# Kernel tuning notes

Hardware: AMD Instinct MI355X
Metric: run time of the kernel (lower is better)

## Reference

```python
import jax, jax.numpy as jnp
import numpy as np

N_NODES = 100000
N_EDGES = 1600000
IN_CH = 128
OUT_CH = 64

def setup_inputs() -> dict:
    key = jax.random.key(0)
    k = jax.random.split(key, 7)
    x = jax.random.normal(k[0], (N_NODES, IN_CH), dtype=jnp.float32)
    edge_index = jax.random.randint(k[1], (2, N_EDGES), 0, N_NODES, dtype=jnp.int64)
    neg_edge_index = jax.random.randint(k[2], (2, N_EDGES), 0, N_NODES, dtype=jnp.int64)
    # GCNConv weight [in, out] + bias, Linear classifier [2*out, 2] + bias
    W = jax.random.normal(k[3], (IN_CH, OUT_CH), dtype=jnp.float32) / np.sqrt(IN_CH)
    b = jnp.zeros((OUT_CH,), dtype=jnp.float32)
    Wc = jax.random.normal(k[4], (2 * OUT_CH, 2), dtype=jnp.float32) / np.sqrt(2 * OUT_CH)
    bc = jnp.zeros((2,), dtype=jnp.float32)
    return {"x": x, "edge_index": edge_index, "neg_edge_index": neg_edge_index,
            "W": W, "b": b, "Wc": Wc, "bc": bc}

def reference(x, edge_index, neg_edge_index, W, b, Wc, bc):
    N = x.shape[0]
    # --- GCNConv: linear transform, add self-loops, symmetric deg normalization ---
    h = x @ W                                   # [N, out]
    loops = jnp.arange(N, dtype=edge_index.dtype)
    row = jnp.concatenate([edge_index[0], loops])   # source
    col = jnp.concatenate([edge_index[1], loops])   # target
    deg = jax.ops.segment_sum(jnp.ones(col.shape, h.dtype), col, num_segments=N)
    dinv = jnp.where(deg > 0, jax.lax.rsqrt(deg), 0.0)
    norm = dinv[row] * dinv[col]                # [E+N]
    agg = jax.ops.segment_sum(h[row] * norm[:, None], col, num_segments=N)
    z = jax.nn.relu(agg + b)                    # [N, out]
    # --- edge feature gather (pos + neg edges) + linear classifier ---
    total = jnp.concatenate([edge_index, neg_edge_index], axis=1)  # [2, 2E]
    feats = jnp.concatenate([z[total[0]], z[total[1]]], axis=1)    # [2E, 2*out]
    return feats @ Wc + bc                      # [2E, 2]
```

## Files before the change

kernel.cpp:

```cpp
#include <hip/hip_runtime.h>

#define IN_CH 128
#define OUT_CH 64
#define MAXBKT 256
#define CAPB   9216
#define CAPB_PAD 16896
#define CHUNK  3328

typedef __attribute__((ext_vector_type(8))) short short8v;
typedef __attribute__((ext_vector_type(4))) float float4v;

union Pack { short8v s8; unsigned u[4]; };

__device__ __forceinline__ unsigned short f2bf(float f) {
    unsigned u = __float_as_uint(f);
    return (unsigned short)((u + 0x7fffu + ((u >> 16) & 1u)) >> 16);
}
__device__ __forceinline__ unsigned pk2(float a, float b) {
    return ((unsigned)f2bf(b) << 16) | (unsigned)f2bf(a);
}
__device__ __forceinline__ float bflo(unsigned d) { return __uint_as_float(d << 16); }
__device__ __forceinline__ float bfhi(unsigned d) { return __uint_as_float(d & 0xffff0000u); }

__global__ void k_zero_cnt(unsigned* __restrict__ cnt, int n) {
    int i = blockIdx.x * blockDim.x + threadIdx.x;
    if (i < n) cnt[i] = 0u;
}

__global__ __launch_bounds__(256) void k_binA(const int* __restrict__ ei,
                                              unsigned* __restrict__ bucketCount,
                                              unsigned* __restrict__ binned,
                                              int E, int nbkt) {
    __shared__ unsigned hist[MAXBKT];
    __shared__ unsigned resv[MAXBKT];
    __shared__ int colS[CHUNK];
    int tid = threadIdx.x;
    int start = blockIdx.x * CHUNK;
    int end = start + CHUNK; if (end > E) end = E;
    int cnt = end - start;

    for (int i = tid; i < MAXBKT; i += 256) hist[i] = 0u;
    __syncthreads();

    for (int i = tid; i < cnt; i += 256) {
        int c = ei[E + start + i];
        colS[i] = c;
        atomicAdd(&hist[c >> 9], 1u);
    }
    __syncthreads();

    if (tid < nbkt) {
        resv[tid] = atomicAdd(&bucketCount[tid], hist[tid]);
        hist[tid] = 0u;
    }
    __syncthreads();

    for (int i = tid; i < cnt; i += 256) {
        int c = colS[i];
        int r = ei[start + i];
        int bkt = c >> 9;
        unsigned rank = atomicAdd(&hist[bkt], 1u);
        unsigned idx = resv[bkt] + rank;
        if (idx < CAPB)
            binned[(size_t)bkt * CAPB + idx] = ((unsigned)r << 9) | (unsigned)(c & 511);
    }
}

__global__ __launch_bounds__(1024) void k_csrB(const unsigned* __restrict__ binned,
                                               const unsigned* __restrict__ bucketCount,
                                               int* __restrict__ rows,
                                               unsigned* __restrict__ offs,
                                               unsigned* __restrict__ degPad,
                                               float* __restrict__ dinv, int N, int nbkt) {
    __shared__ unsigned hist[512];
    __shared__ unsigned excl[512];
    __shared__ unsigned wsum[8];
    __shared__ unsigned wexc[8];
    __shared__ unsigned stage[CAPB];
    int tid = threadIdx.x;
    int b = blockIdx.x;
    unsigned cnt = bucketCount[b];
    if (cnt > (unsigned)CAPB) cnt = (unsigned)CAPB;
    size_t gbase = (size_t)b * CAPB_PAD;
    int nodeBase = b << 9;
    int nn = N - nodeBase; if (nn > 512) nn = 512;

    for (int i = tid; i < 512; i += 1024) hist[i] = 0u;
    __syncthreads();

    const unsigned* src = binned + (size_t)b * CAPB;
    for (unsigned i = tid; i < cnt; i += 1024) {
        unsigned p = src[i];
        stage[i] = p;
        atomicAdd(&hist[p & 511u], 1u);
    }
    __syncthreads();

    unsigned d = 0, dp = 0, winc = 0;
    if (tid < 512) {
        d = hist[tid];
        dp = (d + 15u) & ~15u;
        winc = dp;
#pragma unroll
        for (int o = 1; o < 64; o <<= 1) {
            unsigned t = __shfl_up(winc, o);
            if ((tid & 63) >= o) winc += t;
        }
        if ((tid & 63) == 63) wsum[tid >> 6] = winc;
    }
    __syncthreads();
    if (tid < 8) {
        unsigned s = wsum[tid];
        unsigned inc = s;
#pragma unroll
        for (int o = 1; o < 8; o <<= 1) {
            unsigned t = __shfl_up(inc, o);
            if (tid >= o) inc += t;
        }
        wexc[tid] = inc - s;
    }
    __syncthreads();
    if (tid < 512) excl[tid] = wexc[tid >> 6] + winc - dp;
    __syncthreads();

    if (tid < nn) {
        offs[nodeBase + tid]   = (unsigned)gbase + excl[tid];
        degPad[nodeBase + tid] = dp;
        dinv[nodeBase + tid]   = rsqrtf((float)d + 1.0f);
    }

    for (unsigned i = tid; i < cnt; i += 1024) {
        unsigned p = stage[i];
        unsigned c = p & 511u;
        unsigned r = atomicAdd(&hist[c], 0xFFFFFFFFu);
        rows[gbase + excl[c] + r - 1u] = (int)(p >> 9);
    }
    if (tid < nn) {
        size_t base = gbase + excl[tid];
        for (unsigned p = d; p < dp; ++p) rows[base + p] = N;
    }
}

__global__ __launch_bounds__(256) void k_gemm_h(const float* __restrict__ x,
                                                const float* __restrict__ W,
                                                const float* __restrict__ dinv,
                                                unsigned short* __restrict__ hs,
                                                int N, int nChunks) {
    __shared__ float Wl[IN_CH * 66];
    int tid = threadIdx.x;
    int wid = tid >> 6;
    int l   = tid & 63;
    int g   = l >> 4;
    int m   = l & 15;

    if (blockIdx.x == 0 && tid < 32)
        ((unsigned*)hs)[((size_t)N << 5) + tid] = 0u;

    const float4* W4 = (const float4*)W;
#pragma unroll
    for (int j = 0; j < 8; ++j) {
        int i4 = tid + j * 256;
        float4 w = W4[i4];
        int i = i4 * 4;
        int k = i >> 6, c = i & 63;
        float* dst = Wl + k * 66 + c;
        dst[0] = w.x; dst[1] = w.y; dst[2] = w.z; dst[3] = w.w;
    }
    __syncthreads();

    short8v bf[4][4];
#pragma unroll
    for (int s = 0; s < 4; ++s)
#pragma unroll
        for (int t = 0; t < 4; ++t) {
            Pack p;
#pragma unroll
            for (int jj = 0; jj < 4; ++jj) {
                int k = s * 32 + g * 8 + 2 * jj;
                float f0 = Wl[(k + 0) * 66 + t * 16 + m];
                float f1 = Wl[(k + 1) * 66 + t * 16 + m];
                p.u[jj] = pk2(f0, f1);
            }
            bf[s][t] = p.s8;
        }

    const float4* x4 = (const float4*)x;
    for (int chunk = blockIdx.x; chunk < nChunks; chunk += gridDim.x) {
        int R0 = chunk * 64 + wid * 16;
        int rowA = R0 + m; if (rowA > N - 1) rowA = N - 1;
        float4v acc[4];
#pragma unroll
        for (int t = 0; t < 4; ++t) acc[t] = (float4v){0.f, 0.f, 0.f, 0.f};

#pragma unroll
        for (int s = 0; s < 4; ++s) {
            const float4* ap = x4 + (size_t)rowA * 32 + s * 8 + g * 2;
            float4 a0 = ap[0];
            float4 a1 = ap[1];
            Pack pa;
            pa.u[0] = pk2(a0.x, a0.y);
            pa.u[1] = pk2(a0.z, a0.w);
            pa.u[2] = pk2(a1.x, a1.y);
            pa.u[3] = pk2(a1.z, a1.w);
#pragma unroll
            for (int t = 0; t < 4; ++t)
                acc[t] = __builtin_amdgcn_mfma_f32_16x16x32_bf16(pa.s8, bf[s][t], acc[t], 0, 0, 0);
        }

        int rbase = R0 + g * 4;
        float4 dv = *(const float4*)(dinv + rbase);
#pragma unroll
        for (int r = 0; r < 4; ++r) {
            int row = rbase + r;
            if (row < N) {
                float dvr = (r == 0) ? dv.x : (r == 1) ? dv.y : (r == 2) ? dv.z : dv.w;
#pragma unroll
                for (int t = 0; t < 4; ++t)
                    hs[(size_t)row * OUT_CH + t * 16 + m] = f2bf(acc[t][r] * dvr);
            }
        }
    }
}

__global__ __launch_bounds__(256) void k_gather(const unsigned* __restrict__ offs,
                                                const unsigned* __restrict__ degPad,
                                                const int* __restrict__ rows,
                                                const unsigned* __restrict__ hsd,
                                                const float* __restrict__ dinv,
                                                const float* __restrict__ b,
                                                const float* __restrict__ Wc,
                                                float* __restrict__ u,
                                                float* __restrict__ v, int n) {
    int lane = threadIdx.x & 63;
    int half = lane >> 5;
    int l32  = lane & 31;
    int node = blockIdx.x * (blockDim.x >> 6) + (threadIdx.x >> 6);
    if (node >= n) return;
    unsigned start = offs[node];
    unsigned cntP = degPad[node];
    const int* rp = rows + start;

    unsigned ds = hsd[((size_t)node << 5) + l32];
    float acc0 = half ? 0.f : bflo(ds);
    float acc1 = half ? 0.f : bfhi(ds);

    for (unsigned j0 = 0; j0 < cntP; j0 += 64) {
        unsigned rem = cntP - j0;
        unsigned np = rem < 64u ? rem : 64u;
        int myidx = rp[j0 + (lane < (int)np ? lane : 0)];

        for (unsigned t0 = 0; t0 < np; t0 += 16) {
            int rr[8];
#pragma unroll
            for (int s = 0; s < 8; ++s)
                rr[s] = __shfl(myidx, (int)t0 + 2 * s + half);
            unsigned dd[8];
#pragma unroll
            for (int s = 0; s < 8; ++s)
                dd[s] = hsd[((size_t)rr[s] << 5) + l32];
#pragma unroll
            for (int s = 0; s < 8; ++s) {
                acc0 += bflo(dd[s]);
                acc1 += bfhi(dd[s]);
            }
        }
    }

    acc0 += __shfl_xor(acc0, 32);
    acc1 += __shfl_xor(acc1, 32);

    float di = dinv[node];
    float2 bv = ((const float2*)b)[l32];
    float z0 = fmaxf(fmaf(acc0, di, bv.x), 0.f);
    float z1 = fmaxf(fmaf(acc1, di, bv.y), 0.f);

    float4 w = ((const float4*)(Wc + (half ? 128 : 0)))[l32];
    float p0 = z0 * w.x + z1 * w.z;
    float p1 = z0 * w.y + z1 * w.w;
#pragma unroll
    for (int off = 16; off > 0; off >>= 1) {
        p0 += __shfl_xor(p0, off);
        p1 += __shfl_xor(p1, off);
    }
    float2 r; r.x = p0; r.y = p1;
    if (lane == 0)  ((float2*)u)[node] = r;
    if (lane == 32) ((float2*)v)[node] = r;
}

__global__ void k_edges(const int* __restrict__ ei, const int* __restrict__ nei,
                        const float* __restrict__ u, const float* __restrict__ v,
                        const float* __restrict__ bc, float* __restrict__ out, int E) {
    int i = blockIdx.x * blockDim.x + threadIdx.x;
    int quads = E >> 1;
    if (i >= quads) return;
    int halfQ = quads >> 1;
    const int* base = (i < halfQ) ? ei : nei;
    int pi = (i < halfQ) ? i : i - halfQ;
    int4 ss = ((const int4*)base)[pi];
    int4 dd = ((const int4*)(base + E))[pi];
    float2 u0 = ((const float2*)u)[ss.x];
    float2 u1 = ((const float2*)u)[ss.y];
    float2 u2 = ((const float2*)u)[ss.z];
    float2 u3 = ((const float2*)u)[ss.w];
    float2 v0 = ((const float2*)v)[dd.x];
    float2 v1 = ((const float2*)v)[dd.y];
    float2 v2 = ((const float2*)v)[dd.z];
    float2 v3 = ((const float2*)v)[dd.w];
    float b0 = bc[0], b1 = bc[1];
    float4 r0, r1;
    r0.x = u0.x + v0.x + b0;  r0.y = u0.y + v0.y + b1;
    r0.z = u1.x + v1.x + b0;  r0.w = u1.y + v1.y + b1;
    r1.x = u2.x + v2.x + b0;  r1.y = u2.y + v2.y + b1;
    r1.z = u3.x + v3.x + b0;  r1.w = u3.y + v3.y + b1;
    ((float4*)out)[2 * i + 0] = r0;
    ((float4*)out)[2 * i + 1] = r1;
}

extern "C" void kernel_launch(void* const* d_in, const int* in_sizes, int n_in,
                              void* d_out, int out_size, void* d_ws, size_t ws_size,
                              hipStream_t stream) {
    const float* x   = (const float*)d_in[0];
    const int*   ei  = (const int*)d_in[1];
    const int*   nei = (const int*)d_in[2];
    const float* W   = (const float*)d_in[3];
    const float* b   = (const float*)d_in[4];
    const float* Wc  = (const float*)d_in[5];
    const float* bc  = (const float*)d_in[6];
    float* out = (float*)d_out;

    const int N = in_sizes[0] / IN_CH;
    const int E = in_sizes[1] / 2;
    const int nbkt = (N + 511) >> 9;
    const int nChunks = (N + 63) / 64;

    char* ws = (char*)d_ws;
    size_t off = 0;
    unsigned short* hs = (unsigned short*)(ws + off); off += ((size_t)N + 1) * OUT_CH * 2;
    unsigned* binned = (unsigned*)(ws + off); off += (size_t)MAXBKT * CAPB * 4;
    int*      rows   = (int*)(ws + off);      off += (size_t)MAXBKT * CAPB_PAD * 4;
    unsigned* offs   = (unsigned*)(ws + off); off += (size_t)N * 4;
    unsigned* degP   = (unsigned*)(ws + off); off += (size_t)N * 4;
    float*    dinv   = (float*)(ws + off);    off += (size_t)N * 4;
    float*    u      = (float*)(ws + off);    off += (size_t)N * 2 * 4;
    float*    v      = (float*)(ws + off);    off += (size_t)N * 2 * 4;
    unsigned* bucketCount = (unsigned*)(ws + off); off += (size_t)MAXBKT * 4;

    k_zero_cnt<<<1, 256, 0, stream>>>(bucketCount, MAXBKT);
    k_binA<<<(E + CHUNK - 1) / CHUNK, 256, 0, stream>>>(ei, bucketCount, binned, E, nbkt);
    k_csrB<<<nbkt, 1024, 0, stream>>>(binned, bucketCount, rows, offs, degP, dinv, N, nbkt);
    k_gemm_h<<<512, 256, 0, stream>>>(x, W, dinv, hs, N, nChunks);
    k_gather<<<(N + 3) / 4, 256, 0, stream>>>(offs, degP, rows, (const unsigned*)hs, dinv, b, Wc, u, v, N);
    k_edges<<<(E / 2 + 255) / 256, 256, 0, stream>>>(ei, nei, u, v, bc, out, E);
}
```

Before: 137.7 us.

## Fuse edge binning with GEMM and defer dinv scaling into CSR kernel

Edge binning and the x@W GEMM now run in one launch, with blocks split by index, so the two independent stages overlap and one kernel launch goes away. Because the GEMM no longer waits for dinv, it writes unscaled bf16 h, and the CSR kernel rescales each node's row by dinv after computing degrees. The cost is an extra read-modify-write pass over hs in the CSR kernel and a second bf16 rounding. The GEMM also drops its grid-stride loop and launches one block per 64-row chunk, which repacks the W fragments in every block.

```diff
diff --git a/kernel.cpp b/kernel.cpp
--- a/kernel.cpp
+++ b/kernel.cpp
@@ -27,42 +27,120 @@
     if (i < n) cnt[i] = 0u;
 }
 
-__global__ __launch_bounds__(256) void k_binA(const int* __restrict__ ei,
-                                              unsigned* __restrict__ bucketCount,
-                                              unsigned* __restrict__ binned,
-                                              int E, int nbkt) {
-    __shared__ unsigned hist[MAXBKT];
-    __shared__ unsigned resv[MAXBKT];
-    __shared__ int colS[CHUNK];
+__global__ __launch_bounds__(256) void k_AG(const float* __restrict__ x,
+                                            const float* __restrict__ W,
+                                            const int* __restrict__ ei,
+                                            unsigned* __restrict__ bucketCount,
+                                            unsigned* __restrict__ binned,
+                                            unsigned short* __restrict__ hs,
+                                            int N, int E, int nbkt, int nBin) {
+    __shared__ float smem[IN_CH * 66];
     int tid = threadIdx.x;
-    int start = blockIdx.x * CHUNK;
-    int end = start + CHUNK; if (end > E) end = E;
-    int cnt = end - start;
-
-    for (int i = tid; i < MAXBKT; i += 256) hist[i] = 0u;
-    __syncthreads();
-
-    for (int i = tid; i < cnt; i += 256) {
-        int c = ei[E + start + i];
-        colS[i] = c;
-        atomicAdd(&hist[c >> 9], 1u);
-    }
-    __syncthreads();
-
-    if (tid < nbkt) {
-        resv[tid] = atomicAdd(&bucketCount[tid], hist[tid]);
-        hist[tid] = 0u;
-    }
-    __syncthreads();
-
-    for (int i = tid; i < cnt; i += 256) {
-        int c = colS[i];
-        int r = ei[start + i];
-        int bkt = c >> 9;
-        unsigned rank = atomicAdd(&hist[bkt], 1u);
-        unsigned idx = resv[bkt] + rank;
-        if (idx < CAPB)
-            binned[(size_t)bkt * CAPB + idx] = ((unsigned)r << 9) | (unsigned)(c & 511);
+
+    if (blockIdx.x < nBin) {
+        unsigned* hist = (unsigned*)smem;
+        unsigned* resv = hist + MAXBKT;
+        int* colS = (int*)(resv + MAXBKT);
+        int start = blockIdx.x * CHUNK;
+        int end = start + CHUNK; if (end > E) end = E;
+        int cnt = end - start;
+
+        for (int i = tid; i < MAXBKT; i += 256) hist[i] = 0u;
+        __syncthreads();
+
+        for (int i = tid; i < cnt; i += 256) {
+            int c = ei[E + start + i];
+            colS[i] = c;
+            atomicAdd(&hist[c >> 9], 1u);
+        }
+        __syncthreads();
+
+        if (tid < nbkt) {
+            resv[tid] = atomicAdd(&bucketCount[tid], hist[tid]);
+            hist[tid] = 0u;
+        }
+        __syncthreads();
+
+        for (int i = tid; i < cnt; i += 256) {
+            int c = colS[i];
+            int r = ei[start + i];
+            int bkt = c >> 9;
+            unsigned rank = atomicAdd(&hist[bkt], 1u);
+            unsigned idx = resv[bkt] + rank;
+            if (idx < CAPB)
+                binned[(size_t)bkt * CAPB + idx] = ((unsigned)r << 9) | (unsigned)(c & 511);
+        }
+    } else {
+        int chunk = blockIdx.x - nBin;
+        int wid = tid >> 6;
+        int l   = tid & 63;
+        int g   = l >> 4;
+        int m   = l & 15;
+
+        if (chunk == 0 && tid < 32)
+            ((unsigned*)hs)[((size_t)N << 5) + tid] = 0u;
+
+        float* Wl = smem;
+        const float4* W4 = (const float4*)W;
+#pragma unroll
+        for (int j = 0; j < 8; ++j) {
+            int i4 = tid + j * 256;
+            float4 w = W4[i4];
+            int i = i4 * 4;
+            int k = i >> 6, c = i & 63;
+            float* dst = Wl + k * 66 + c;
+            dst[0] = w.x; dst[1] = w.y; dst[2] = w.z; dst[3] = w.w;
+        }
+        __syncthreads();
+
+        short8v bf[4][4];
+#pragma unroll
+        for (int s = 0; s < 4; ++s)
+#pragma unroll
+            for (int t = 0; t < 4; ++t) {
+                Pack p;
+#pragma unroll
+                for (int jj = 0; jj < 4; ++jj) {
+                    int k = s * 32 + g * 8 + 2 * jj;
+                    float f0 = Wl[(k + 0) * 66 + t * 16 + m];
+                    float f1 = Wl[(k + 1) * 66 + t * 16 + m];
+                    p.u[jj] = pk2(f0, f1);
+                }
+                bf[s][t] = p.s8;
+            }
+
+        int R0 = chunk * 64 + wid * 16;
+        int rowA = R0 + m; if (rowA > N - 1) rowA = N - 1;
+        float4v acc[4];
+#pragma unroll
+        for (int t = 0; t < 4; ++t) acc[t] = (float4v){0.f, 0.f, 0.f, 0.f};
+
+        const float4* x4 = (const float4*)x;
+#pragma unroll
+        for (int s = 0; s < 4; ++s) {
+            const float4* ap = x4 + (size_t)rowA * 32 + s * 8 + g * 2;
+            float4 a0 = ap[0];
+            float4 a1 = ap[1];
+            Pack pa;
+            pa.u[0] = pk2(a0.x, a0.y);
+            pa.u[1] = pk2(a0.z, a0.w);
+            pa.u[2] = pk2(a1.x, a1.y);
+            pa.u[3] = pk2(a1.z, a1.w);
+#pragma unroll
+            for (int t = 0; t < 4; ++t)
+                acc[t] = __builtin_amdgcn_mfma_f32_16x16x32_bf16(pa.s8, bf[s][t], acc[t], 0, 0, 0);
+        }
+
+        int rbase = R0 + g * 4;
+#pragma unroll
+        for (int r = 0; r < 4; ++r) {
+            int row = rbase + r;
+            if (row < N) {
+#pragma unroll
+                for (int t = 0; t < 4; ++t)
+                    hs[(size_t)row * OUT_CH + t * 16 + m] = f2bf(acc[t][r]);
+            }
+        }
     }
 }
 
@@ -71,8 +149,11 @@
                                                int* __restrict__ rows,
                                                unsigned* __restrict__ offs,
                                                unsigned* __restrict__ degPad,
-                                               float* __restrict__ dinv, int N, int nbkt) {
+                                               float* __restrict__ dinv,
+                                               unsigned short* __restrict__ hs,
+                                               int N, int nbkt) {
     __shared__ unsigned hist[512];
+    __shared__ unsigned degS[512];
     __shared__ unsigned excl[512];
     __shared__ unsigned wsum[8];
     __shared__ unsigned wexc[8];
@@ -99,6 +180,7 @@
     unsigned d = 0, dp = 0, winc = 0;
     if (tid < 512) {
         d = hist[tid];
+        degS[tid] = d;
         dp = (d + 15u) & ~15u;
         winc = dp;
 #pragma unroll
@@ -139,85 +221,20 @@
         size_t base = gbase + excl[tid];
         for (unsigned p = d; p < dp; ++p) rows[base + p] = N;
     }
-}
-
-__global__ __launch_bounds__(256) void k_gemm_h(const float* __restrict__ x,
-                                                const float* __restrict__ W,
-                                                const float* __restrict__ dinv,
-                                                unsigned short* __restrict__ hs,
-                                                int N, int nChunks) {
-    __shared__ float Wl[IN_CH * 66];
-    int tid = threadIdx.x;
-    int wid = tid >> 6;
-    int l   = tid & 63;
-    int g   = l >> 4;
-    int m   = l & 15;
-
-    if (blockIdx.x == 0 && tid < 32)
-        ((unsigned*)hs)[((size_t)N << 5) + tid] = 0u;
-
-    const float4* W4 = (const float4*)W;
-#pragma unroll
-    for (int j = 0; j < 8; ++j) {
-        int i4 = tid + j * 256;
-        float4 w = W4[i4];
-        int i = i4 * 4;
-        int k = i >> 6, c = i & 63;
-        float* dst = Wl + k * 66 + c;
-        dst[0] = w.x; dst[1] = w.y; dst[2] = w.z; dst[3] = w.w;
-    }
-    __syncthreads();
-
-    short8v bf[4][4];
-#pragma unroll
-    for (int s = 0; s < 4; ++s)
-#pragma unroll
-        for (int t = 0; t < 4; ++t) {
-            Pack p;
-#pragma unroll
-            for (int jj = 0; jj < 4; ++jj) {
-                int k = s * 32 + g * 8 + 2 * jj;
-                float f0 = Wl[(k + 0) * 66 + t * 16 + m];
-                float f1 = Wl[(k + 1) * 66 + t * 16 + m];
-                p.u[jj] = pk2(f0, f1);
-            }
-            bf[s][t] = p.s8;
-        }
-
-    const float4* x4 = (const float4*)x;
-    for (int chunk = blockIdx.x; chunk < nChunks; chunk += gridDim.x) {
-        int R0 = chunk * 64 + wid * 16;
-        int rowA = R0 + m; if (rowA > N - 1) rowA = N - 1;
-        float4v acc[4];
-#pragma unroll
-        for (int t = 0; t < 4; ++t) acc[t] = (float4v){0.f, 0.f, 0.f, 0.f};
-
-#pragma unroll
-        for (int s = 0; s < 4; ++s) {
-            const float4* ap = x4 + (size_t)rowA * 32 + s * 8 + g * 2;
-            float4 a0 = ap[0];
-            float4 a1 = ap[1];
-            Pack pa;
-            pa.u[0] = pk2(a0.x, a0.y);
-            pa.u[1] = pk2(a0.z, a0.w);
-            pa.u[2] = pk2(a1.x, a1.y);
-            pa.u[3] = pk2(a1.z, a1.w);
-#pragma unroll
-            for (int t = 0; t < 4; ++t)
-                acc[t] = __builtin_amdgcn_mfma_f32_16x16x32_bf16(pa.s8, bf[s][t], acc[t], 0, 0, 0);
-        }
-
-        int rbase = R0 + g * 4;
-        float4 dv = *(const float4*)(dinv + rbase);
-#pragma unroll
-        for (int r = 0; r < 4; ++r) {
-            int row = rbase + r;
-            if (row < N) {
-                float dvr = (r == 0) ? dv.x : (r == 1) ? dv.y : (r == 2) ? dv.z : dv.w;
-#pragma unroll
-                for (int t = 0; t < 4; ++t)
-                    hs[(size_t)row * OUT_CH + t * 16 + m] = f2bf(acc[t][r] * dvr);
-            }
+
+    int node_l = tid >> 1;
+    if (node_l < nn) {
+        float dv = rsqrtf((float)degS[node_l] + 1.0f);
+        uint4* hq = (uint4*)hs;
+        size_t base = ((size_t)(nodeBase + node_l) << 3) + ((size_t)(tid & 1) << 2);
+#pragma unroll
+        for (int q = 0; q < 4; ++q) {
+            uint4 w = hq[base + q];
+            w.x = pk2(bflo(w.x) * dv, bfhi(w.x) * dv);
+            w.y = pk2(bflo(w.y) * dv, bfhi(w.y) * dv);
+            w.z = pk2(bflo(w.z) * dv, bfhi(w.z) * dv);
+            w.w = pk2(bflo(w.w) * dv, bfhi(w.w) * dv);
+            hq[base + q] = w;
         }
     }
 }
@@ -332,6 +349,7 @@
     const int E = in_sizes[1] / 2;
     const int nbkt = (N + 511) >> 9;
     const int nChunks = (N + 63) / 64;
+    const int nBin = (E + CHUNK - 1) / CHUNK;
 
     char* ws = (char*)d_ws;
     size_t off = 0;
@@ -346,9 +364,8 @@
     unsigned* bucketCount = (unsigned*)(ws + off); off += (size_t)MAXBKT * 4;
 
     k_zero_cnt<<<1, 256, 0, stream>>>(bucketCount, MAXBKT);
-    k_binA<<<(E + CHUNK - 1) / CHUNK, 256, 0, stream>>>(ei, bucketCount, binned, E, nbkt);
-    k_csrB<<<nbkt, 1024, 0, stream>>>(binned, bucketCount, rows, offs, degP, dinv, N, nbkt);
-    k_gemm_h<<<512, 256, 0, stream>>>(x, W, dinv, hs, N, nChunks);
+    k_AG<<<nBin + nChunks, 256, 0, stream>>>(x, W, ei, bucketCount, binned, hs, N, E, nbkt, nBin);
+    k_csrB<<<nbkt, 1024, 0, stream>>>(binned, bucketCount, rows, offs, degP, dinv, hs, N, nbkt);
     k_gather<<<(N + 3) / 4, 256, 0, stream>>>(offs, degP, rows, (const unsigned*)hs, dinv, b, Wc, u, v, N);
     k_edges<<<(E / 2 + 255) / 256, 256, 0, stream>>>(ei, nei, u, v, bc, out, E);
 }
```

New measurement: 132.2 us. 4.0% less time.
